# Optimization experiments

Hardware: AMD Instinct MI355X
Metric: run time of the kernel (lower is better)

The kernel has to match this reference:

```python
import jax, jax.numpy as jnp
import numpy as np

N = 100000   # num nodes
E = 1600000  # num edges
D = 128      # input_dim
K = 5        # APPNP propagation steps
EPS = 1e-8   # torch cosine_similarity eps


def setup_inputs() -> dict:
    key = jax.random.key(0)
    k1, k2, k3, k4 = jax.random.split(key, 4)
    x = jax.random.normal(k1, (N, D), jnp.float32)
    mask = jax.random.normal(k2, (N, 1), jnp.float32)
    edge_index = jax.random.randint(k3, (2, E), 0, N, dtype=jnp.int32)
    # init_t: orthogonal weight with gain sqrt(2), zero bias
    W = jax.nn.initializers.orthogonal(scale=2 ** 0.5)(k4, (D, D), jnp.float32)
    b = jnp.zeros((D,), jnp.float32)
    alpha = jnp.array(0.5, jnp.float32)
    return {"x": x, "mask": mask, "edge_index": edge_index, "W": W, "b": b, "alpha": alpha}


def reference(x, mask, edge_index, W, b, alpha):
    n = x.shape[0]
    # x_fn: Linear + Tanh
    h = jnp.tanh(x @ W.T + b)
    src, dst = edge_index[0], edge_index[1]
    hs, hd = h[src], h[dst]  # [E, D] gathers
    # torch F.cosine_similarity with eps-clamped norms
    dot = jnp.sum(hs * hd, axis=-1)
    ns = jnp.maximum(jnp.sqrt(jnp.sum(hs * hs, axis=-1)), EPS)
    nd = jnp.maximum(jnp.sqrt(jnp.sum(hd * hd, axis=-1)), EPS)
    edge_weights = jax.nn.relu(dot / (ns * nd))  # [E]

    fill = jax.nn.relu(mask)  # [N, 1]

    # PyG APPNP: gcn_norm with self loops (fill value 1.0)
    loops = jnp.arange(n, dtype=src.dtype)
    row = jnp.concatenate([src, loops])
    col = jnp.concatenate([dst, loops])
    w = jnp.concatenate([edge_weights, jnp.ones((n,), edge_weights.dtype)])
    deg = jax.ops.segment_sum(w, col, num_segments=n)
    dinv = jnp.where(deg > 0, jax.lax.rsqrt(jnp.maximum(deg, EPS)), 0.0)
    norm = dinv[row] * w * dinv[col]  # [E+N]

    # K-step APPNP: z <- (1-alpha) * A_hat z + alpha * fill
    z = fill
    for _ in range(K):
        agg = jax.ops.segment_sum(norm[:, None] * z[row], col, num_segments=n)
        z = (1.0 - alpha) * agg + alpha * fill
    return z, edge_weights
```

## Files before the change

kernel.cpp:

```cpp
#include <hip/hip_runtime.h>
#include <hip/hip_bf16.h>

typedef __attribute__((ext_vector_type(2))) float f32x2;
typedef __attribute__((ext_vector_type(4))) float f32x4;
typedef __attribute__((ext_vector_type(8))) short short8;

#define D 128
#define EPS 1e-8f
#define BSH 8
#define BSZ 256
#define SMAX 8000
#define OSH 12
#define OBK 4096

__device__ __forceinline__ short f2bf(float f) {
    unsigned int u = __float_as_uint(f);
    unsigned int r = (u + 0x7fffu + ((u >> 16) & 1u)) >> 16;
    return (short)r;
}

__device__ __forceinline__ unsigned int pkbf(float lo, float hi) {
    unsigned int r;
    asm("v_cvt_pk_bf16_f32 %0, %1, %2" : "=v"(r) : "v"(lo), "v"(hi));
    return r;
}

__device__ __forceinline__ float ftanh(float y) {
    float e = __builtin_amdgcn_exp2f(y * 2.885390082f);
    float r = __builtin_amdgcn_rcpf(e + 1.0f);
    return __builtin_fmaf(-2.0f, r, 1.0f);
}

__device__ __forceinline__ int dot4(unsigned int a, unsigned int b, int c) {
#if __has_builtin(__builtin_amdgcn_sdot4)
    return __builtin_amdgcn_sdot4((int)a, (int)b, c, false);
#else
    int r = c;
    r += (int)(char)(a) * (int)(char)(b);
    r += (int)(char)(a >> 8) * (int)(char)(b >> 8);
    r += (int)(char)(a >> 16) * (int)(char)(b >> 16);
    r += (int)(char)(a >> 24) * (int)(char)(b >> 24);
    return r;
#endif
}

__global__ __launch_bounds__(256) void cvinit_kernel(const float* __restrict__ W,
                                                     short* __restrict__ Wbf,
                                                     const float* __restrict__ mask,
                                                     float* __restrict__ fill, int N) {
    int i = blockIdx.x * 256 + threadIdx.x;
    if (i < N) fill[i] = fmaxf(mask[i], 0.0f);
    if (i < D * D) Wbf[i] = f2bf(W[i]);
}

__global__ __launch_bounds__(256) void gemm_kernel(const float* __restrict__ x,
                                                   const short* __restrict__ Wbf,
                                                   const float* __restrict__ b,
                                                   signed char* __restrict__ hn8,
                                                   int N) {
    int tid  = threadIdx.x;
    int wave = tid >> 6;
    int lane = tid & 63;
    int l16  = lane & 15;
    int g    = lane >> 4;
    int r0   = blockIdx.x * 64 + wave * 16;

    int arow = r0 + l16;
    if (arow >= N) arow = N - 1;
    union { uint4 u; short8 s; } afr[4];
#pragma unroll
    for (int kc = 0; kc < 4; ++kc) {
        const float* xp = x + (size_t)arow * D + kc * 32 + g * 8;
        float4 lo = *(const float4*)xp;
        float4 hi = *(const float4*)(xp + 4);
        afr[kc].u.x = pkbf(lo.x, lo.y);
        afr[kc].u.y = pkbf(lo.z, lo.w);
        afr[kc].u.z = pkbf(hi.x, hi.y);
        afr[kc].u.w = pkbf(hi.z, hi.w);
    }

    f32x4 acc[8];
#pragma unroll
    for (int j = 0; j < 8; ++j) acc[j] = (f32x4){0.f, 0.f, 0.f, 0.f};

#pragma unroll
    for (int j = 0; j < 8; ++j) {
#pragma unroll
        for (int kc = 0; kc < 4; ++kc) {
            const short8* bp =
                (const short8*)(Wbf + ((size_t)(j * 16 + l16) * D + kc * 32 + g * 8));
            acc[j] = __builtin_amdgcn_mfma_f32_16x16x32_bf16(afr[kc].s, *bp, acc[j], 0, 0, 0);
        }
    }

    float tt[8][4];
    float sq[4] = {0.f, 0.f, 0.f, 0.f};
#pragma unroll
    for (int j = 0; j < 8; ++j) {
        float bj = b[j * 16 + l16];
#pragma unroll
        for (int r = 0; r < 4; ++r) {
            float t = ftanh(acc[j][r] + bj);
            tt[j][r] = t;
            sq[r] = __builtin_fmaf(t, t, sq[r]);
        }
    }
#pragma unroll
    for (int m = 1; m <= 8; m <<= 1) {
#pragma unroll
        for (int r = 0; r < 4; ++r) sq[r] += __shfl_xor(sq[r], m);
    }
    float inv[4];
#pragma unroll
    for (int r = 0; r < 4; ++r) inv[r] = rsqrtf(fmaxf(sq[r], 1e-16f)) * 127.0f;

#pragma unroll
    for (int r = 0; r < 4; ++r) {
        int row = r0 + g * 4 + r;
        if (row < N) {
#pragma unroll
            for (int j = 0; j < 8; ++j) {
                hn8[(size_t)row * D + j * 16 + l16] =
                    (signed char)__float2int_rn(tt[j][r] * inv[r]);
            }
        }
    }
}

__global__ __launch_bounds__(256) void bcnt_kernel(const int* __restrict__ dst,
                                                   int* __restrict__ M,
                                                   int E, int nbk, int nblk, int chunk) {
    extern __shared__ int cnt[];
    int b = blockIdx.x;
    for (int k = threadIdx.x; k < nbk; k += 256) cnt[k] = 0;
    __syncthreads();
    int beg = b * chunk, end = min(E, beg + chunk);
    for (int e = beg + threadIdx.x; e < end; e += 256)
        atomicAdd(&cnt[dst[e] >> BSH], 1);
    __syncthreads();
    for (int k = threadIdx.x; k < nbk; k += 256)
        M[k * nblk + b] = cnt[k];
}

__global__ __launch_bounds__(1024) void scan_blk(const int* __restrict__ cnt,
                                                 int* __restrict__ rp,
                                                 int* __restrict__ bsum, int nq) {
    __shared__ int wsum[16];
    __shared__ int sexcl[16];
    int tid = threadIdx.x, lane = tid & 63, wv = tid >> 6;
    int idx = blockIdx.x * 1024 + tid;
    int4 c = (idx < nq) ? ((const int4*)cnt)[idx] : make_int4(0, 0, 0, 0);
    int tsum = c.x + c.y + c.z + c.w;
    int incl = tsum;
#pragma unroll
    for (int m = 1; m < 64; m <<= 1) {
        int t = __shfl_up(incl, m);
        if (lane >= m) incl += t;
    }
    if (lane == 63) wsum[wv] = incl;
    __syncthreads();
    if (tid == 0) {
        int acc = 0;
#pragma unroll
        for (int k = 0; k < 16; ++k) { int t = wsum[k]; sexcl[k] = acc; acc += t; }
        bsum[blockIdx.x] = acc;
    }
    __syncthreads();
    int excl = sexcl[wv] + incl - tsum;
    if (idx < nq) {
        int4 r;
        r.x = excl; r.y = excl + c.x; r.z = r.y + c.y; r.w = r.z + c.z;
        ((int4*)rp)[idx] = r;
    }
}

__global__ __launch_bounds__(256) void scan_top(int* __restrict__ bsum,
                                                int* __restrict__ boff, int nbs,
                                                int* __restrict__ gcur, int nbk2) {
    for (int k = threadIdx.x; k < nbk2; k += 256) gcur[k] = k << OSH;
    if (threadIdx.x == 0) {
        int acc = 0;
        for (int k = 0; k < nbs; ++k) { int t = bsum[k]; boff[k] = acc; acc += t; }
    }
}

__global__ __launch_bounds__(256) void scan_add(int* __restrict__ data,
                                                const int* __restrict__ boff, int nq) {
    int idx = blockIdx.x * 256 + threadIdx.x;
    if (idx < nq) {
        int off = boff[idx >> 10];
        int4 r = ((int4*)data)[idx];
        r.x += off; r.y += off; r.z += off; r.w += off;
        ((int4*)data)[idx] = r;
    }
}

__global__ __launch_bounds__(256) void bscat_kernel(const int* __restrict__ src,
                                                    const int* __restrict__ dst,
                                                    const int* __restrict__ Mo,
                                                    int2* __restrict__ ebuf,
                                                    int E, int nbk, int nblk, int chunk) {
    extern __shared__ int cur[];
    int b = blockIdx.x;
    for (int k = threadIdx.x; k < nbk; k += 256) cur[k] = Mo[k * nblk + b];
    __syncthreads();
    int beg = b * chunk, end = min(E, beg + chunk);
    for (int e = beg + threadIdx.x; e < end; e += 256) {
        int d = dst[e];
        int k = d >> BSH;
        int p = atomicAdd(&cur[k], 1);
        ebuf[p] = make_int2(src[e], (e << BSH) | (d & (BSZ - 1)));
    }
}

__global__ __launch_bounds__(256) void binsort_kernel(const int* __restrict__ Mo,
                                                      const int2* __restrict__ ebuf,
                                                      int* __restrict__ esrc,
                                                      int* __restrict__ eorig,
                                                      int* __restrict__ rp,
                                                      int E, int N, int nbk, int nblk) {
    extern __shared__ char smem[];
    int2* stage = (int2*)smem;
    int*  cnt   = (int*)(smem + SMAX * 8);
    int k = blockIdx.x;
    int base = Mo[k * nblk];
    int endb = (k + 1 < nbk) ? Mo[(k + 1) * nblk] : E;
    int m = endb - base;
    if (m > SMAX) m = SMAX;

    if (threadIdx.x < BSZ) cnt[threadIdx.x] = 0;
    __syncthreads();
    for (int i = threadIdx.x; i < m; i += 256) {
        int2 v = ebuf[base + i];
        stage[i] = v;
        atomicAdd(&cnt[v.y & (BSZ - 1)], 1);
    }
    __syncthreads();
    if (threadIdx.x == 0) {
        int acc = 0;
#pragma unroll 8
        for (int t = 0; t < BSZ; ++t) { int c = cnt[t]; cnt[t] = acc; acc += c; }
    }
    __syncthreads();
    {
        int node = (k << BSH) + threadIdx.x;
        if (threadIdx.x < BSZ && node < N) rp[node] = base + cnt[threadIdx.x];
        if (k == nbk - 1 && threadIdx.x == 0) rp[N] = E;
    }
    __syncthreads();
    for (int i = threadIdx.x; i < m; i += 256) {
        int2 v = stage[i];
        int p = atomicAdd(&cnt[v.y & (BSZ - 1)], 1);
        esrc[base + p]  = v.x;
        eorig[base + p] = v.y >> BSH;
    }
}

__global__ __launch_bounds__(256) void weight_kernel(const int* __restrict__ rp,
                                                     const int* __restrict__ esrc,
                                                     const signed char* __restrict__ hn8,
                                                     float* __restrict__ warr,
                                                     float* __restrict__ deg, int N) {
    const float SC = 1.0f / 16129.0f;
    int gid = (blockIdx.x * 256 + threadIdx.x) >> 3;
    int l   = threadIdx.x & 7;
    if (gid >= N) return;
    const uint4* hp = (const uint4*)hn8;
    uint4 dv = hp[(size_t)gid * 8 + l];
    int beg = rp[gid], end = rp[gid + 1];
    float sum = 0.f;
    int s = beg;
    for (; s + 3 < end; s += 4) {
        int i0 = esrc[s], i1 = esrc[s + 1], i2 = esrc[s + 2], i3 = esrc[s + 3];
        uint4 u0 = hp[(size_t)i0 * 8 + l];
        uint4 u1 = hp[(size_t)i1 * 8 + l];
        uint4 u2 = hp[(size_t)i2 * 8 + l];
        uint4 u3 = hp[(size_t)i3 * 8 + l];
        int d0 = dot4(u0.x, dv.x, 0); d0 = dot4(u0.y, dv.y, d0);
        d0 = dot4(u0.z, dv.z, d0);    d0 = dot4(u0.w, dv.w, d0);
        int d1 = dot4(u1.x, dv.x, 0); d1 = dot4(u1.y, dv.y, d1);
        d1 = dot4(u1.z, dv.z, d1);    d1 = dot4(u1.w, dv.w, d1);
        int d2 = dot4(u2.x, dv.x, 0); d2 = dot4(u2.y, dv.y, d2);
        d2 = dot4(u2.z, dv.z, d2);    d2 = dot4(u2.w, dv.w, d2);
        int d3 = dot4(u3.x, dv.x, 0); d3 = dot4(u3.y, dv.y, d3);
        d3 = dot4(u3.z, dv.z, d3);    d3 = dot4(u3.w, dv.w, d3);
#pragma unroll
        for (int m = 4; m >= 1; m >>= 1) {
            d0 += __shfl_xor(d0, m); d1 += __shfl_xor(d1, m);
            d2 += __shfl_xor(d2, m); d3 += __shfl_xor(d3, m);
        }
        float w0 = fmaxf((float)d0 * SC, 0.f), w1 = fmaxf((float)d1 * SC, 0.f);
        float w2 = fmaxf((float)d2 * SC, 0.f), w3 = fmaxf((float)d3 * SC, 0.f);
        if (l == 0) { warr[s] = w0; warr[s + 1] = w1; warr[s + 2] = w2; warr[s + 3] = w3; }
        sum += (w0 + w1) + (w2 + w3);
    }
    for (; s < end; ++s) {
        int i0 = esrc[s];
        uint4 u0 = hp[(size_t)i0 * 8 + l];
        int d0 = dot4(u0.x, dv.x, 0); d0 = dot4(u0.y, dv.y, d0);
        d0 = dot4(u0.z, dv.z, d0);    d0 = dot4(u0.w, dv.w, d0);
#pragma unroll
        for (int m = 4; m >= 1; m >>= 1) d0 += __shfl_xor(d0, m);
        float w0 = fmaxf((float)d0 * SC, 0.f);
        if (l == 0) warr[s] = w0;
        sum += w0;
    }
    if (l == 0) deg[gid] = 1.0f + sum;
}

__global__ __launch_bounds__(256) void dscat_kernel(const int* __restrict__ eorig,
                                                    const float* __restrict__ warr,
                                                    int* __restrict__ gcur,
                                                    int2* __restrict__ pbuf,
                                                    int E, int nbk2, int chunk) {
    extern __shared__ char smem[];
    int2* stage = (int2*)smem;
    int*  hist  = (int*)(smem + (size_t)chunk * 8);
    int*  lcur  = hist + nbk2;
    int b = blockIdx.x;
    for (int k = threadIdx.x; k < nbk2; k += 256) hist[k] = 0;
    __syncthreads();
    int beg = b * chunk, end = min(E, beg + chunk), m = end - beg;
    for (int i = threadIdx.x; i < m; i += 256) {
        int o = eorig[beg + i];
        float w = warr[beg + i];
        stage[i] = make_int2(o, __float_as_int(w));
        atomicAdd(&hist[o >> OSH], 1);
    }
    __syncthreads();
    for (int k = threadIdx.x; k < nbk2; k += 256) {
        int c = hist[k];
        lcur[k] = c ? atomicAdd(&gcur[k], c) : 0;
    }
    __syncthreads();
    for (int i = threadIdx.x; i < m; i += 256) {
        int2 v = stage[i];
        int p = atomicAdd(&lcur[v.x >> OSH], 1);
        pbuf[p] = v;
    }
}

__global__ __launch_bounds__(256) void dfin_kernel(const int2* __restrict__ pbuf,
                                                   float* __restrict__ ew, int E,
                                                   const float* __restrict__ deg,
                                                   float* __restrict__ dinv, int N) {
    int i = blockIdx.x * 256 + threadIdx.x;
    if (i < N) {
        float dg = deg[i];
        dinv[i] = (dg > 0.f) ? rsqrtf(fmaxf(dg, EPS)) : 0.f;
    }
    int base = blockIdx.x << OSH;
    int m = min(OBK, E - base);
    for (int t = threadIdx.x; t < m; t += 256) {
        int2 v = pbuf[base + t];
        ew[v.x] = __int_as_float(v.y);
    }
}

__global__ __launch_bounds__(256) void appnp_first_kernel(const int* __restrict__ rp,
                                                          const int* __restrict__ esrc,
                                                          const float* __restrict__ warr,
                                                          float* __restrict__ wfin,
                                                          const float* __restrict__ dinv,
                                                          const float* __restrict__ fill,
                                                          const float* __restrict__ alpha,
                                                          float* __restrict__ zout, int N) {
    int t = blockIdx.x * 256 + threadIdx.x;
    int i = t >> 2, l = t & 3;
    if (i >= N) return;
    int beg = rp[i], end = rp[i + 1];
    float al = alpha[0];
    float oma = 1.0f - al;
    float di = dinv[i];
    float s = 0.f;
    for (int j = beg + l; j < end; j += 4) {
        int sr = esrc[j];
        float wf = oma * warr[j] * di * dinv[sr];
        wfin[j] = wf;
        s += wf * fill[sr];
    }
    s += __shfl_xor(s, 1);
    s += __shfl_xor(s, 2);
    if (l == 0) {
        float fi = fill[i];
        zout[i] = al * fi + oma * di * di * fi + s;
    }
}

__global__ __launch_bounds__(256) void appnp_kernel(const int* __restrict__ rp,
                                                    const int* __restrict__ esrc,
                                                    const float* __restrict__ wfin,
                                                    const float* __restrict__ dinv,
                                                    const float* __restrict__ fill,
                                                    const float* __restrict__ zin,
                                                    const float* __restrict__ alpha,
                                                    float* __restrict__ zout, int N) {
    int t = blockIdx.x * 256 + threadIdx.x;
    int i = t >> 2, l = t & 3;
    if (i >= N) return;
    int beg = rp[i], end = rp[i + 1];
    float s = 0.f;
    for (int j = beg + l; j < end; j += 4)
        s += wfin[j] * zin[esrc[j]];
    s += __shfl_xor(s, 1);
    s += __shfl_xor(s, 2);
    if (l == 0) {
        float al = alpha[0];
        float di = dinv[i];
        zout[i] = al * fill[i] + (1.0f - al) * di * di * zin[i] + s;
    }
}

extern "C" void kernel_launch(void* const* d_in, const int* in_sizes, int n_in,
                              void* d_out, int out_size, void* d_ws, size_t ws_size,
                              hipStream_t stream) {
    const float* x     = (const float*)d_in[0];
    const float* mask  = (const float*)d_in[1];
    const int*   ei    = (const int*)d_in[2];
    const float* W     = (const float*)d_in[3];
    const float* b     = (const float*)d_in[4];
    const float* alpha = (const float*)d_in[5];

    int N = in_sizes[1];
    int E = in_sizes[2] / 2;
    const int* src = ei;
    const int* dst = ei + E;

    float* out = (float*)d_out;
    float* ew  = out + N;

    int Np = (N + 15) & ~15;

    int NBK  = (N + BSZ - 1) >> BSH;
    int NBLK = 400;
    int CHUNK = (E + NBLK - 1) / NBLK;
    int L = NBK * NBLK;

    int NBK2   = (E + OBK - 1) >> OSH;
    int NBLK2  = 400;
    int CHUNK2 = (E + NBLK2 - 1) / NBLK2;

    char* wsb = (char*)d_ws;
    signed char* hn8 = (signed char*)wsb;
    int2* pbuf = (int2*)wsb;
    char* p = wsb + (size_t)N * D;
    short* Wbf  = (short*)p;           p += (size_t)D * D * 2;
    float* deg  = (float*)p;           p += (size_t)Np * 4;
    float* dinv = (float*)p;           p += (size_t)Np * 4;
    float* fill = (float*)p;           p += (size_t)Np * 4;
    float* zA   = (float*)p;           p += (size_t)Np * 4;
    float* zB   = (float*)p;           p += (size_t)Np * 4;
    int*   rp   = (int*)p;             p += (size_t)(Np + 16) * 4;
    int*   M    = (int*)p;             p += (size_t)L * 4;
    int*   Mo   = (int*)p;             p += (size_t)(L + 16) * 4;
    int*   bsum = (int*)p;             p += 64 * 4;
    int*   boff = (int*)p;             p += 64 * 4;
    int*   gcur = (int*)p;             p += 512 * 4;
    int2*  ebuf = (int2*)p;            p += (size_t)E * 8;
    int*   esrc = (int*)p;             p += (size_t)E * 4;
    int*   eorig= (int*)p;             p += (size_t)E * 4;
    float* warr = (float*)p;
    float* wfin = (float*)eorig;

    int nb_n = (N + 255) / 256;
    int nb_n4 = ((size_t)N * 4 + 255) / 256;
    int nq   = L / 4;
    int nbs  = (nq + 1023) / 1024;
    int ldsA = ((NBK * 4) + 15) & ~15;
    int ldsB = SMAX * 8 + BSZ * 4;
    int ldsD = CHUNK2 * 8 + 2 * NBK2 * 4;

    cvinit_kernel<<<nb_n, 256, 0, stream>>>(W, Wbf, mask, fill, N);
    gemm_kernel<<<(N + 63) / 64, 256, 0, stream>>>(x, Wbf, b, hn8, N);

    bcnt_kernel<<<NBLK, 256, ldsA, stream>>>(dst, M, E, NBK, NBLK, CHUNK);
    scan_blk<<<nbs, 1024, 0, stream>>>(M, Mo, bsum, nq);
    scan_top<<<1, 256, 0, stream>>>(bsum, boff, nbs, gcur, NBK2);
    scan_add<<<(nq + 255) / 256, 256, 0, stream>>>(Mo, boff, nq);
    bscat_kernel<<<NBLK, 256, ldsA, stream>>>(src, dst, Mo, ebuf, E, NBK, NBLK, CHUNK);
    binsort_kernel<<<NBK, 256, ldsB, stream>>>(Mo, ebuf, esrc, eorig, rp, E, N, NBK, NBLK);

    weight_kernel<<<((size_t)N * 8 + 255) / 256, 256, 0, stream>>>(rp, esrc, hn8, warr, deg, N);

    dscat_kernel<<<NBLK2, 256, ldsD, stream>>>(eorig, warr, gcur, pbuf, E, NBK2, CHUNK2);
    dfin_kernel<<<NBK2, 256, 0, stream>>>(pbuf, ew, E, deg, dinv, N);

    appnp_first_kernel<<<nb_n4, 256, 0, stream>>>(rp, esrc, warr, wfin, dinv, fill, alpha, zA, N);
    appnp_kernel<<<nb_n4, 256, 0, stream>>>(rp, esrc, wfin, dinv, fill, zA, alpha, zB, N);
    appnp_kernel<<<nb_n4, 256, 0, stream>>>(rp, esrc, wfin, dinv, fill, zB, alpha, zA, N);
    appnp_kernel<<<nb_n4, 256, 0, stream>>>(rp, esrc, wfin, dinv, fill, zA, alpha, zB, N);
    appnp_kernel<<<nb_n4, 256, 0, stream>>>(rp, esrc, wfin, dinv, fill, zB, alpha, out, N);
}
```

Measured before the change: 239.6 us.

## Make GEMM kernel persistent with software-prefetched x tiles

The tanh-linear GEMM kernel now runs on a fixed grid of 768 blocks. Each wave loops over 16-row tiles in grid-stride fashion and loads the next tile's x rows into registers while computing the current tile's MFMAs. Bias values are hoisted out of the loop. The aim is to hide global load latency and reduce block launch overhead. In exchange it raises register pressure and may lower occupancy, and it is only one of many kernels in the pipeline.

```diff
diff --git a/kernel.cpp b/kernel.cpp
--- a/kernel.cpp
+++ b/kernel.cpp
@@ -12,6 +12,7 @@
 #define SMAX 8000
 #define OSH 12
 #define OBK 4096
+#define GEMM_BLOCKS 768
 
 __device__ __forceinline__ short f2bf(float f) {
     unsigned int u = __float_as_uint(f);
@@ -63,65 +64,84 @@
     int lane = tid & 63;
     int l16  = lane & 15;
     int g    = lane >> 4;
-    int r0   = blockIdx.x * 64 + wave * 16;
-
-    int arow = r0 + l16;
-    if (arow >= N) arow = N - 1;
-    union { uint4 u; short8 s; } afr[4];
-#pragma unroll
-    for (int kc = 0; kc < 4; ++kc) {
-        const float* xp = x + (size_t)arow * D + kc * 32 + g * 8;
-        float4 lo = *(const float4*)xp;
-        float4 hi = *(const float4*)(xp + 4);
-        afr[kc].u.x = pkbf(lo.x, lo.y);
-        afr[kc].u.y = pkbf(lo.z, lo.w);
-        afr[kc].u.z = pkbf(hi.x, hi.y);
-        afr[kc].u.w = pkbf(hi.z, hi.w);
-    }
-
-    f32x4 acc[8];
-#pragma unroll
-    for (int j = 0; j < 8; ++j) acc[j] = (f32x4){0.f, 0.f, 0.f, 0.f};
-
-#pragma unroll
-    for (int j = 0; j < 8; ++j) {
+    int ntiles = (N + 15) >> 4;
+    int wt = blockIdx.x * 4 + wave;
+    int ws = gridDim.x * 4;
+
+    float bj[8];
+#pragma unroll
+    for (int j = 0; j < 8; ++j) bj[j] = b[j * 16 + l16];
+
+    float4 rlo[4], rhi[4];
+    if (wt < ntiles) {
+        int ar = wt * 16 + l16; if (ar >= N) ar = N - 1;
+        const float* xp = x + (size_t)ar * D + g * 8;
 #pragma unroll
         for (int kc = 0; kc < 4; ++kc) {
-            const short8* bp =
-                (const short8*)(Wbf + ((size_t)(j * 16 + l16) * D + kc * 32 + g * 8));
-            acc[j] = __builtin_amdgcn_mfma_f32_16x16x32_bf16(afr[kc].s, *bp, acc[j], 0, 0, 0);
-        }
-    }
-
-    float tt[8][4];
-    float sq[4] = {0.f, 0.f, 0.f, 0.f};
-#pragma unroll
-    for (int j = 0; j < 8; ++j) {
-        float bj = b[j * 16 + l16];
+            rlo[kc] = *(const float4*)(xp + kc * 32);
+            rhi[kc] = *(const float4*)(xp + kc * 32 + 4);
+        }
+    }
+
+    for (int t = wt; t < ntiles; t += ws) {
+        union { uint4 u; short8 s; } afr[4];
+#pragma unroll
+        for (int kc = 0; kc < 4; ++kc) {
+            afr[kc].u.x = pkbf(rlo[kc].x, rlo[kc].y);
+            afr[kc].u.y = pkbf(rlo[kc].z, rlo[kc].w);
+            afr[kc].u.z = pkbf(rhi[kc].x, rhi[kc].y);
+            afr[kc].u.w = pkbf(rhi[kc].z, rhi[kc].w);
+        }
+        int tn = t + ws;
+        if (tn < ntiles) {
+            int ar = tn * 16 + l16; if (ar >= N) ar = N - 1;
+            const float* xp = x + (size_t)ar * D + g * 8;
+#pragma unroll
+            for (int kc = 0; kc < 4; ++kc) {
+                rlo[kc] = *(const float4*)(xp + kc * 32);
+                rhi[kc] = *(const float4*)(xp + kc * 32 + 4);
+            }
+        }
+
+        f32x4 acc[8];
+#pragma unroll
+        for (int j = 0; j < 8; ++j) acc[j] = (f32x4){0.f, 0.f, 0.f, 0.f};
+#pragma unroll
+        for (int j = 0; j < 8; ++j) {
+#pragma unroll
+            for (int kc = 0; kc < 4; ++kc) {
+                const short8* bp =
+                    (const short8*)(Wbf + ((size_t)(j * 16 + l16) * D + kc * 32 + g * 8));
+                acc[j] = __builtin_amdgcn_mfma_f32_16x16x32_bf16(afr[kc].s, *bp, acc[j], 0, 0, 0);
+            }
+        }
+
+        float sq[4] = {0.f, 0.f, 0.f, 0.f};
+#pragma unroll
+        for (int j = 0; j < 8; ++j) {
+#pragma unroll
+            for (int r = 0; r < 4; ++r) {
+                float tt = ftanh(acc[j][r] + bj[j]);
+                acc[j][r] = tt;
+                sq[r] = __builtin_fmaf(tt, tt, sq[r]);
+            }
+        }
+#pragma unroll
+        for (int m = 1; m <= 8; m <<= 1) {
+#pragma unroll
+            for (int r = 0; r < 4; ++r) sq[r] += __shfl_xor(sq[r], m);
+        }
+        int r0 = t * 16;
 #pragma unroll
         for (int r = 0; r < 4; ++r) {
-            float t = ftanh(acc[j][r] + bj);
-            tt[j][r] = t;
-            sq[r] = __builtin_fmaf(t, t, sq[r]);
-        }
-    }
-#pragma unroll
-    for (int m = 1; m <= 8; m <<= 1) {
-#pragma unroll
-        for (int r = 0; r < 4; ++r) sq[r] += __shfl_xor(sq[r], m);
-    }
-    float inv[4];
-#pragma unroll
-    for (int r = 0; r < 4; ++r) inv[r] = rsqrtf(fmaxf(sq[r], 1e-16f)) * 127.0f;
-
-#pragma unroll
-    for (int r = 0; r < 4; ++r) {
-        int row = r0 + g * 4 + r;
-        if (row < N) {
-#pragma unroll
-            for (int j = 0; j < 8; ++j) {
-                hn8[(size_t)row * D + j * 16 + l16] =
-                    (signed char)__float2int_rn(tt[j][r] * inv[r]);
+            float inv = rsqrtf(fmaxf(sq[r], 1e-16f)) * 127.0f;
+            int row = r0 + g * 4 + r;
+            if (row < N) {
+#pragma unroll
+                for (int j = 0; j < 8; ++j) {
+                    hn8[(size_t)row * D + j * 16 + l16] =
+                        (signed char)__float2int_rn(acc[j][r] * inv);
+                }
             }
         }
     }
@@ -471,7 +491,7 @@
     int ldsD = CHUNK2 * 8 + 2 * NBK2 * 4;
 
     cvinit_kernel<<<nb_n, 256, 0, stream>>>(W, Wbf, mask, fill, N);
-    gemm_kernel<<<(N + 63) / 64, 256, 0, stream>>>(x, Wbf, b, hn8, N);
+    gemm_kernel<<<GEMM_BLOCKS, 256, 0, stream>>>(x, Wbf, b, hn8, N);
 
     bcnt_kernel<<<NBLK, 256, ldsA, stream>>>(dst, M, E, NBK, NBLK, CHUNK);
     scan_blk<<<nbs, 1024, 0, stream>>>(M, Mo, bsum, nq);
```

New measurement: 241.5 us. Within noise of the previous version (+0.8%).
